# Optimization experiments

Measured on AMD Instinct MI355X. Metric: run time of the kernel, lower is better.

Reference implementation:

```python
import jax, jax.numpy as jnp
import numpy as np

EPS = 1e-6

def feature_map(x):
    # 'elu' feature map: elu(x) + 1 (positive feature map from Katharopoulos et al.)
    return jax.nn.elu(x) + 1.0

def setup_inputs() -> dict:
    key = jax.random.key(0)
    kq, kk, kv = jax.random.split(key, 3)
    B, L, H, D = 4, 2048, 16, 64
    q = jax.random.normal(kq, (B, L, H, D), dtype=jnp.float32)
    k = jax.random.normal(kk, (B, L, H, D), dtype=jnp.float32)
    v = jax.random.normal(kv, (B, L, H, D), dtype=jnp.float32)
    return {"q": q, "k": k, "v": v}

def reference(q, k, v):
    # q, k, v: [N, L, H, D]  (attention_mask=None -> causal linear attention)
    qf = feature_map(q)
    kf = feature_map(k)
    # normalizer: z[n,l,h] = sum_d qf[n,l,h,d] * cumsum_s<=l kf[n,s,h,d]
    z = jnp.einsum('nlhd,nlhd->nlh', qf, jnp.cumsum(kf, axis=1)) + EPS
    # causal_dot_product via scan over sequence with carry S[n,h,d,m]
    B, L, H, D = q.shape
    M = v.shape[-1]
    qs = jnp.moveaxis(qf, 1, 0)  # [L, N, H, D]
    ks = jnp.moveaxis(kf, 1, 0)
    vs = jnp.moveaxis(v, 1, 0)

    def step(S, qkv):
        ql, kl, vl = qkv                              # [N,H,D], [N,H,D], [N,H,M]
        S = S + jnp.einsum('nhd,nhm->nhdm', kl, vl)   # running sum of k v^T
        out = jnp.einsum('nhd,nhdm->nhm', ql, S)
        return S, out

    S0 = jnp.zeros((B, H, D, M), dtype=q.dtype)
    _, outs = jax.lax.scan(step, S0, (qs, ks, vs))    # outs: [L, N, H, M]
    v_ = jnp.moveaxis(outs, 0, 1)                     # [N, L, H, M]
    return v_ / z[..., None]
```

## Files before the change

### kernel.cpp

```cpp
#include <hip/hip_runtime.h>
#include <cstdint>

#define LL 2048
#define HH 16
#define DD 64
#define NC 32
#define LSTR 1024
#define EPSF 1e-6f
#define PAD 72

typedef __bf16 bf16x8 __attribute__((ext_vector_type(8)));
typedef float floatx4 __attribute__((ext_vector_type(4)));
typedef unsigned short ushortx8 __attribute__((ext_vector_type(8)));
typedef unsigned short ushortx4 __attribute__((ext_vector_type(4)));
typedef unsigned short ushortx2 __attribute__((ext_vector_type(2)));

static __device__ __forceinline__ float fmap(float x){ return x > 0.f ? x + 1.f : __expf(x); }
static __device__ __forceinline__ unsigned short f2bf(float f){
    unsigned u = __builtin_bit_cast(unsigned, f);
    u += 0x7fffu + ((u >> 16) & 1u);
    return (unsigned short)(u >> 16);
}
static __device__ __forceinline__ float bf2f(unsigned short s){
    unsigned u = ((unsigned)s) << 16;
    return __builtin_bit_cast(float, u);
}
static __device__ __forceinline__ bf16x8 ldf(const unsigned short* p){
    return __builtin_bit_cast(bf16x8, *(const ushortx8*)p);
}

__global__ __launch_bounds__(256) void k1(const float* __restrict__ kp, const float* __restrict__ vp,
                                          unsigned short* __restrict__ kvt, float* __restrict__ ks)
{
    __shared__ __align__(16) unsigned short kft[DD*PAD];
    __shared__ __align__(16) unsigned short vtt[DD*PAD];
    const int ci = blockIdx.x;
    const int c = ci & 31, bh = ci >> 5, b = bh >> 4, h = bh & 15;
    const int t = threadIdx.x;
    const int64_t gbase = ((int64_t)(b*LL + c*DD)*HH + h)*DD;
#pragma unroll
    for (int i = 0; i < 2; ++i) {
        int flat = t + 256*i;
        int l0 = (flat >> 4) * 2, col = (flat & 15) << 2;
        const float* gk = kp + gbase + (int64_t)l0*LSTR + col;
        const float* gv = vp + gbase + (int64_t)l0*LSTR + col;
        float4 ka = *(const float4*)(gk);
        float4 kb = *(const float4*)(gk + LSTR);
        float4 va = *(const float4*)(gv);
        float4 vb = *(const float4*)(gv + LSTR);
        float kaa[4] = {ka.x,ka.y,ka.z,ka.w}, kbb[4] = {kb.x,kb.y,kb.z,kb.w};
        float vaa[4] = {va.x,va.y,va.z,va.w}, vbb[4] = {vb.x,vb.y,vb.z,vb.w};
#pragma unroll
        for (int e = 0; e < 4; ++e) {
            *(ushortx2*)(kft + (col+e)*PAD + l0) = ushortx2{ f2bf(fmap(kaa[e])), f2bf(fmap(kbb[e])) };
            *(ushortx2*)(vtt + (col+e)*PAD + l0) = ushortx2{ f2bf(vaa[e]), f2bf(vbb[e]) };
        }
    }
    __syncthreads();
    const int w = t >> 6, lane = t & 63, quad = lane >> 4, lr = lane & 15;
    const int m0 = 16*w;
    floatx4 acc[4];
#pragma unroll
    for (int dt = 0; dt < 4; ++dt) acc[dt] = floatx4{0.f,0.f,0.f,0.f};
#pragma unroll
    for (int kk = 0; kk < 2; ++kk) {
        bf16x8 a = ldf(vtt + (m0+lr)*PAD + kk*32 + quad*8);
#pragma unroll
        for (int dt = 0; dt < 4; ++dt) {
            bf16x8 bb = ldf(kft + (dt*16+lr)*PAD + kk*32 + quad*8);
            acc[dt] = __builtin_amdgcn_mfma_f32_16x16x32_bf16(a, bb, acc[dt], 0, 0, 0);
        }
    }
    unsigned short* kvo = kvt + (int64_t)ci*4096;
#pragma unroll
    for (int dt = 0; dt < 4; ++dt)
#pragma unroll
        for (int r = 0; r < 4; ++r)
            kvo[(m0 + quad*4 + r)*DD + dt*16 + lr] = f2bf(acc[dt][r]);
    if (t < DD) {
        float s = 0.f;
#pragma unroll
        for (int j = 0; j < 8; ++j) {
            ushortx8 u = *(const ushortx8*)(kft + t*PAD + j*8);
#pragma unroll
            for (int e = 0; e < 8; ++e) s += bf2f(u[e]);
        }
        ks[(int64_t)ci*DD + t] = s;
    }
}

__global__ __launch_bounds__(256) void k2(unsigned short* __restrict__ kvt, float* __restrict__ ks)
{
    const int blk = blockIdx.x;
    const int bh = blk >> 3, part = blk & 7, t = threadIdx.x;
    unsigned short* base = kvt + (int64_t)bh*NC*4096 + (part*256 + t)*2;
    float r0 = 0.f, r1 = 0.f;
    unsigned x = *(const unsigned*)base;
    for (int c = 0; c < NC-1; ++c) {
        unsigned xn = *(const unsigned*)(base + (int64_t)(c+1)*4096);
        unsigned o = (unsigned)f2bf(r0) | ((unsigned)f2bf(r1) << 16);
        r0 += bf2f((unsigned short)(x & 0xffffu));
        r1 += bf2f((unsigned short)(x >> 16));
        *(unsigned*)(base + (int64_t)c*4096) = o;
        x = xn;
    }
    *(unsigned*)(base + (int64_t)(NC-1)*4096) = (unsigned)f2bf(r0) | ((unsigned)f2bf(r1) << 16);
    if (part == 0 && t < DD) {
        float r = 0.f;
        float* kb = ks + (int64_t)bh*NC*DD + t;
        for (int c = 0; c < NC; ++c) { float xx = kb[(int64_t)c*DD]; kb[(int64_t)c*DD] = r; r += xx; }
    }
}

__global__ __launch_bounds__(256) void k3(const float* __restrict__ qp, const float* __restrict__ kp,
                                          const float* __restrict__ vp,
                                          const unsigned short* __restrict__ kvt,
                                          const float* __restrict__ ks, float* __restrict__ outp)
{
    __shared__ __align__(16) unsigned short qf [DD*PAD];
    __shared__ __align__(16) unsigned short kfx[80*PAD];
    __shared__ __align__(16) unsigned short vtt[DD*PAD];
    __shared__ float zr[DD];
    const int ci = blockIdx.x;
    const int c = ci & 31, bh = ci >> 5, b = bh >> 4, h = bh & 15;
    const int t = threadIdx.x;
    const int64_t gbase = ((int64_t)(b*LL + c*DD)*HH + h)*DD;
    const unsigned short* kvg = kvt + (int64_t)ci*4096;
    const float* ksg = ks + (int64_t)ci*DD;
#pragma unroll
    for (int i = 0; i < 2; ++i) {
        int flat = t + 256*i;
        int l0 = (flat >> 4) * 2, col = (flat & 15) << 2;
        const float* gq = qp + gbase + (int64_t)l0*LSTR + col;
        const float* gk = kp + gbase + (int64_t)l0*LSTR + col;
        const float* gv = vp + gbase + (int64_t)l0*LSTR + col;
        float4 qa = *(const float4*)(gq);
        float4 qb = *(const float4*)(gq + LSTR);
        float4 ka = *(const float4*)(gk);
        float4 kb = *(const float4*)(gk + LSTR);
        float4 va = *(const float4*)(gv);
        float4 vb = *(const float4*)(gv + LSTR);
        *(ushortx4*)(qf + l0*PAD + col)      = ushortx4{ f2bf(fmap(qa.x)), f2bf(fmap(qa.y)), f2bf(fmap(qa.z)), f2bf(fmap(qa.w)) };
        *(ushortx4*)(qf + (l0+1)*PAD + col)  = ushortx4{ f2bf(fmap(qb.x)), f2bf(fmap(qb.y)), f2bf(fmap(qb.z)), f2bf(fmap(qb.w)) };
        *(ushortx4*)(kfx + l0*PAD + col)     = ushortx4{ f2bf(fmap(ka.x)), f2bf(fmap(ka.y)), f2bf(fmap(ka.z)), f2bf(fmap(ka.w)) };
        *(ushortx4*)(kfx + (l0+1)*PAD + col) = ushortx4{ f2bf(fmap(kb.x)), f2bf(fmap(kb.y)), f2bf(fmap(kb.z)), f2bf(fmap(kb.w)) };
        float vaa[4] = {va.x,va.y,va.z,va.w}, vbb[4] = {vb.x,vb.y,vb.z,vb.w};
#pragma unroll
        for (int e = 0; e < 4; ++e)
            *(ushortx2*)(vtt + (col+e)*PAD + l0) = ushortx2{ f2bf(vaa[e]), f2bf(vbb[e]) };
    }
    if (t < 135) *(ushortx8*)(kfx + 65*PAD + t*8) = ushortx8{0,0,0,0,0,0,0,0};
    if (t < DD)  kfx[64*PAD + t] = f2bf(ksg[t]);
    __syncthreads();

    const int w = t >> 6, lane = t & 63, quad = lane >> 4, lr = lane & 15;
    const int l0 = 16*w;
    bf16x8 aq[2];
    aq[0] = ldf(qf + (l0+lr)*PAD + quad*8);
    aq[1] = ldf(qf + (l0+lr)*PAD + 32 + quad*8);
    bf16x8 bs[2][4];
#pragma unroll
    for (int kk = 0; kk < 2; ++kk)
#pragma unroll
        for (int mt = 0; mt < 4; ++mt)
            bs[kk][mt] = ldf(kvg + (mt*16+lr)*DD + kk*32 + quad*8);

    floatx4 sc[5];
#pragma unroll
    for (int tt = 0; tt < 5; ++tt) sc[tt] = floatx4{0.f,0.f,0.f,0.f};
#pragma unroll
    for (int kk = 0; kk < 2; ++kk)
#pragma unroll
        for (int tt = 0; tt < 5; ++tt) {
            bf16x8 bb = ldf(kfx + (tt*16+lr)*PAD + kk*32 + quad*8);
            sc[tt] = __builtin_amdgcn_mfma_f32_16x16x32_bf16(aq[kk], bb, sc[tt], 0, 0, 0);
        }

    float zp[4] = {0.f,0.f,0.f,0.f};
#pragma unroll
    for (int tt = 0; tt < 4; ++tt)
#pragma unroll
        for (int r = 0; r < 4; ++r) {
            int row = l0 + quad*4 + r;
            int col = tt*16 + lr;
            float val = (col <= row) ? sc[tt][r] : 0.f;
            zp[r] += val;
            qf[row*PAD + col] = f2bf(val);
        }
#pragma unroll
    for (int r = 0; r < 4; ++r) zp[r] += (lr == 0) ? sc[4][r] : 0.f;
#pragma unroll
    for (int m = 1; m < 16; m <<= 1)
#pragma unroll
        for (int r = 0; r < 4; ++r) zp[r] += __shfl_xor(zp[r], m, 64);
    if (lr == 0)
#pragma unroll
        for (int r = 0; r < 4; ++r) zr[l0 + quad*4 + r] = 1.f / (zp[r] + EPSF);

    floatx4 oa[4];
#pragma unroll
    for (int mt = 0; mt < 4; ++mt) oa[mt] = floatx4{0.f,0.f,0.f,0.f};
#pragma unroll
    for (int kk = 0; kk < 2; ++kk) {
        bf16x8 a2 = ldf(qf + (l0+lr)*PAD + kk*32 + quad*8);
#pragma unroll
        for (int mt = 0; mt < 4; ++mt) {
            bf16x8 bv = ldf(vtt + (mt*16+lr)*PAD + kk*32 + quad*8);
            oa[mt] = __builtin_amdgcn_mfma_f32_16x16x32_bf16(a2, bv, oa[mt], 0, 0, 0);
        }
    }
#pragma unroll
    for (int kk = 0; kk < 2; ++kk)
#pragma unroll
        for (int mt = 0; mt < 4; ++mt)
            oa[mt] = __builtin_amdgcn_mfma_f32_16x16x32_bf16(aq[kk], bs[kk][mt], oa[mt], 0, 0, 0);
#pragma unroll
    for (int r = 0; r < 4; ++r) {
        int row = l0 + quad*4 + r;
        float rz = zr[row];
#pragma unroll
        for (int mt = 0; mt < 4; ++mt)
            outp[gbase + (int64_t)row*LSTR + mt*16 + lr] = oa[mt][r] * rz;
    }
}

extern "C" void kernel_launch(void* const* d_in, const int* in_sizes, int n_in,
                              void* d_out, int out_size, void* d_ws, size_t ws_size,
                              hipStream_t stream) {
    const float* q = (const float*)d_in[0];
    const float* k = (const float*)d_in[1];
    const float* v = (const float*)d_in[2];
    float* out = (float*)d_out;
    unsigned short* kvt = (unsigned short*)d_ws;
    float* ks = (float*)((char*)d_ws + (size_t)2048*4096*2);
    k1<<<2048, 256, 0, stream>>>(k, v, kvt, ks);
    k2<<<512,  256, 0, stream>>>(kvt, ks);
    k3<<<2048, 256, 0, stream>>>(q, k, v, kvt, ks, out);
}
```

Measured before the change: 156.0 us.

## Stage bf16 k/v LDS images in k1 and async-load them in k3

k1 now writes the bf16 feature-mapped k tile and the transposed bf16 v tile as padded LDS-layout images in workspace. k3 copies these images straight into shared memory with global_load_lds, so it no longer rereads fp32 k and v, recomputes fmap, or transposes them. This halves k3's k/v read bytes and drops its conversion work, at the cost of extra workspace writes in k1. k2 is also changed to issue all chunk loads up front with unrolled loops, and k3 gets a launch-bounds occupancy hint.

Measured after the change: 162.7 us. 1.04x slower.

```diff
diff --git a/kernel.cpp b/kernel.cpp
--- a/kernel.cpp
+++ b/kernel.cpp
@@ -8,6 +8,7 @@
 #define LSTR 1024
 #define EPSF 1e-6f
 #define PAD 72
+#define IMGSZ 4608
 
 typedef __bf16 bf16x8 __attribute__((ext_vector_type(8)));
 typedef float floatx4 __attribute__((ext_vector_type(4)));
@@ -28,9 +29,15 @@
 static __device__ __forceinline__ bf16x8 ldf(const unsigned short* p){
     return __builtin_bit_cast(bf16x8, *(const ushortx8*)p);
 }
+static __device__ __forceinline__ void gl_lds16(const unsigned short* g, unsigned short* l){
+    __builtin_amdgcn_global_load_lds(
+        (const __attribute__((address_space(1))) void*)g,
+        (__attribute__((address_space(3))) void*)l, 16, 0, 0);
+}
 
 __global__ __launch_bounds__(256) void k1(const float* __restrict__ kp, const float* __restrict__ vp,
-                                          unsigned short* __restrict__ kvt, float* __restrict__ ks)
+                                          unsigned short* __restrict__ kvt, float* __restrict__ ks,
+                                          unsigned short* __restrict__ kfimg, unsigned short* __restrict__ vtimg)
 {
     __shared__ __align__(16) unsigned short kft[DD*PAD];
     __shared__ __align__(16) unsigned short vtt[DD*PAD];
@@ -38,6 +45,7 @@
     const int c = ci & 31, bh = ci >> 5, b = bh >> 4, h = bh & 15;
     const int t = threadIdx.x;
     const int64_t gbase = ((int64_t)(b*LL + c*DD)*HH + h)*DD;
+    unsigned short* kfi = kfimg + (int64_t)ci*IMGSZ;
 #pragma unroll
     for (int i = 0; i < 2; ++i) {
         int flat = t + 256*i;
@@ -48,15 +56,25 @@
         float4 kb = *(const float4*)(gk + LSTR);
         float4 va = *(const float4*)(gv);
         float4 vb = *(const float4*)(gv + LSTR);
-        float kaa[4] = {ka.x,ka.y,ka.z,ka.w}, kbb[4] = {kb.x,kb.y,kb.z,kb.w};
+        ushortx4 kra = { f2bf(fmap(ka.x)), f2bf(fmap(ka.y)), f2bf(fmap(ka.z)), f2bf(fmap(ka.w)) };
+        ushortx4 krb = { f2bf(fmap(kb.x)), f2bf(fmap(kb.y)), f2bf(fmap(kb.z)), f2bf(fmap(kb.w)) };
+        *(ushortx4*)(kfi + l0*PAD + col)     = kra;
+        *(ushortx4*)(kfi + (l0+1)*PAD + col) = krb;
         float vaa[4] = {va.x,va.y,va.z,va.w}, vbb[4] = {vb.x,vb.y,vb.z,vb.w};
 #pragma unroll
         for (int e = 0; e < 4; ++e) {
-            *(ushortx2*)(kft + (col+e)*PAD + l0) = ushortx2{ f2bf(fmap(kaa[e])), f2bf(fmap(kbb[e])) };
+            *(ushortx2*)(kft + (col+e)*PAD + l0) = ushortx2{ kra[e], krb[e] };
             *(ushortx2*)(vtt + (col+e)*PAD + l0) = ushortx2{ f2bf(vaa[e]), f2bf(vbb[e]) };
         }
     }
     __syncthreads();
+    unsigned short* vti = vtimg + (int64_t)ci*IMGSZ;
+#pragma unroll
+    for (int i = 0; i < 2; ++i) {
+        int g = t + 256*i;
+        *(ushortx8*)(vti + g*8) = *(const ushortx8*)(vtt + g*8);
+    }
+    if (t < 64) *(ushortx8*)(vti + 4096 + t*8) = *(const ushortx8*)(vtt + 4096 + t*8);
     const int w = t >> 6, lane = t & 63, quad = lane >> 4, lr = lane & 15;
     const int m0 = 16*w;
     floatx4 acc[4];
@@ -94,28 +112,33 @@
     const int blk = blockIdx.x;
     const int bh = blk >> 3, part = blk & 7, t = threadIdx.x;
     unsigned short* base = kvt + (int64_t)bh*NC*4096 + (part*256 + t)*2;
+    unsigned x[NC];
+#pragma unroll
+    for (int c = 0; c < NC; ++c) x[c] = *(const unsigned*)(base + (int64_t)c*4096);
     float r0 = 0.f, r1 = 0.f;
-    unsigned x = *(const unsigned*)base;
-    for (int c = 0; c < NC-1; ++c) {
-        unsigned xn = *(const unsigned*)(base + (int64_t)(c+1)*4096);
+#pragma unroll
+    for (int c = 0; c < NC; ++c) {
         unsigned o = (unsigned)f2bf(r0) | ((unsigned)f2bf(r1) << 16);
-        r0 += bf2f((unsigned short)(x & 0xffffu));
-        r1 += bf2f((unsigned short)(x >> 16));
+        r0 += bf2f((unsigned short)(x[c] & 0xffffu));
+        r1 += bf2f((unsigned short)(x[c] >> 16));
         *(unsigned*)(base + (int64_t)c*4096) = o;
-        x = xn;
-    }
-    *(unsigned*)(base + (int64_t)(NC-1)*4096) = (unsigned)f2bf(r0) | ((unsigned)f2bf(r1) << 16);
+    }
     if (part == 0 && t < DD) {
+        float kr[NC];
+        float* kb = ks + (int64_t)bh*NC*DD + t;
+#pragma unroll
+        for (int c = 0; c < NC; ++c) kr[c] = kb[(int64_t)c*DD];
         float r = 0.f;
-        float* kb = ks + (int64_t)bh*NC*DD + t;
-        for (int c = 0; c < NC; ++c) { float xx = kb[(int64_t)c*DD]; kb[(int64_t)c*DD] = r; r += xx; }
-    }
-}
-
-__global__ __launch_bounds__(256) void k3(const float* __restrict__ qp, const float* __restrict__ kp,
-                                          const float* __restrict__ vp,
-                                          const unsigned short* __restrict__ kvt,
-                                          const float* __restrict__ ks, float* __restrict__ outp)
+#pragma unroll
+        for (int c = 0; c < NC; ++c) { kb[(int64_t)c*DD] = r; r += kr[c]; }
+    }
+}
+
+__global__ __launch_bounds__(256, 4) void k3(const float* __restrict__ qp,
+                                             const unsigned short* __restrict__ kfimg,
+                                             const unsigned short* __restrict__ vtimg,
+                                             const unsigned short* __restrict__ kvt,
+                                             const float* __restrict__ ks, float* __restrict__ outp)
 {
     __shared__ __align__(16) unsigned short qf [DD*PAD];
     __shared__ __align__(16) unsigned short kfx[80*PAD];
@@ -127,33 +150,35 @@
     const int64_t gbase = ((int64_t)(b*LL + c*DD)*HH + h)*DD;
     const unsigned short* kvg = kvt + (int64_t)ci*4096;
     const float* ksg = ks + (int64_t)ci*DD;
+    const int w = t >> 6, lane = t & 63, quad = lane >> 4, lr = lane & 15;
+
+    {
+        const unsigned short* kfi = kfimg + (int64_t)ci*IMGSZ;
+        const unsigned short* vti = vtimg + (int64_t)ci*IMGSZ;
+#pragma unroll
+        for (int seg = 0; seg < 5; ++seg) {
+            int s = w + seg*4;
+            if (s < 18) {
+                const unsigned short* src = (s < 9) ? (kfi + s*512) : (vti + (s-9)*512);
+                unsigned short*       dst = (s < 9) ? (kfx + s*512) : (vtt + (s-9)*512);
+                gl_lds16(src + lane*8, dst);
+            }
+        }
+    }
 #pragma unroll
     for (int i = 0; i < 2; ++i) {
         int flat = t + 256*i;
         int l0 = (flat >> 4) * 2, col = (flat & 15) << 2;
         const float* gq = qp + gbase + (int64_t)l0*LSTR + col;
-        const float* gk = kp + gbase + (int64_t)l0*LSTR + col;
-        const float* gv = vp + gbase + (int64_t)l0*LSTR + col;
         float4 qa = *(const float4*)(gq);
         float4 qb = *(const float4*)(gq + LSTR);
-        float4 ka = *(const float4*)(gk);
-        float4 kb = *(const float4*)(gk + LSTR);
-        float4 va = *(const float4*)(gv);
-        float4 vb = *(const float4*)(gv + LSTR);
-        *(ushortx4*)(qf + l0*PAD + col)      = ushortx4{ f2bf(fmap(qa.x)), f2bf(fmap(qa.y)), f2bf(fmap(qa.z)), f2bf(fmap(qa.w)) };
-        *(ushortx4*)(qf + (l0+1)*PAD + col)  = ushortx4{ f2bf(fmap(qb.x)), f2bf(fmap(qb.y)), f2bf(fmap(qb.z)), f2bf(fmap(qb.w)) };
-        *(ushortx4*)(kfx + l0*PAD + col)     = ushortx4{ f2bf(fmap(ka.x)), f2bf(fmap(ka.y)), f2bf(fmap(ka.z)), f2bf(fmap(ka.w)) };
-        *(ushortx4*)(kfx + (l0+1)*PAD + col) = ushortx4{ f2bf(fmap(kb.x)), f2bf(fmap(kb.y)), f2bf(fmap(kb.z)), f2bf(fmap(kb.w)) };
-        float vaa[4] = {va.x,va.y,va.z,va.w}, vbb[4] = {vb.x,vb.y,vb.z,vb.w};
-#pragma unroll
-        for (int e = 0; e < 4; ++e)
-            *(ushortx2*)(vtt + (col+e)*PAD + l0) = ushortx2{ f2bf(vaa[e]), f2bf(vbb[e]) };
+        *(ushortx4*)(qf + l0*PAD + col)     = ushortx4{ f2bf(fmap(qa.x)), f2bf(fmap(qa.y)), f2bf(fmap(qa.z)), f2bf(fmap(qa.w)) };
+        *(ushortx4*)(qf + (l0+1)*PAD + col) = ushortx4{ f2bf(fmap(qb.x)), f2bf(fmap(qb.y)), f2bf(fmap(qb.z)), f2bf(fmap(qb.w)) };
     }
     if (t < 135) *(ushortx8*)(kfx + 65*PAD + t*8) = ushortx8{0,0,0,0,0,0,0,0};
     if (t < DD)  kfx[64*PAD + t] = f2bf(ksg[t]);
     __syncthreads();
 
-    const int w = t >> 6, lane = t & 63, quad = lane >> 4, lr = lane & 15;
     const int l0 = 16*w;
     bf16x8 aq[2];
     aq[0] = ldf(qf + (l0+lr)*PAD + quad*8);
@@ -231,9 +256,12 @@
     const float* k = (const float*)d_in[1];
     const float* v = (const float*)d_in[2];
     float* out = (float*)d_out;
-    unsigned short* kvt = (unsigned short*)d_ws;
-    float* ks = (float*)((char*)d_ws + (size_t)2048*4096*2);
-    k1<<<2048, 256, 0, stream>>>(k, v, kvt, ks);
+    char* ws = (char*)d_ws;
+    unsigned short* kvt   = (unsigned short*)ws;
+    float*          ks    = (float*)(ws + (size_t)2048*4096*2);
+    unsigned short* kfimg = (unsigned short*)(ws + (size_t)17*1024*1024);
+    unsigned short* vtimg = kfimg + (size_t)2048*IMGSZ;
+    k1<<<2048, 256, 0, stream>>>(k, v, kvt, ks, kfimg, vtimg);
     k2<<<512,  256, 0, stream>>>(kvt, ks);
-    k3<<<2048, 256, 0, stream>>>(q, k, v, kvt, ks, out);
-}
+    k3<<<2048, 256, 0, stream>>>(q, kfimg, vtimg, kvt, ks, out);
+}
```
